# Optimization experiments

Hardware: AMD Instinct MI355X
Metric: run time of the kernel (lower is better)

Reference implementation:

```python
import jax, jax.numpy as jnp
import numpy as np

N_NODES = 50000
IN_CH = 128
HID = 128
N_EDGES = 800000


def _glorot(key, shape):
    fan_in, fan_out = shape[0], shape[1]
    lim = (6.0 / (fan_in + fan_out)) ** 0.5
    return jax.random.uniform(key, shape, jnp.float32, -lim, lim)


def setup_inputs() -> dict:
    key = jax.random.key(0)
    ks = jax.random.split(key, 8)
    x = jax.random.normal(ks[0], (N_NODES, IN_CH), jnp.float32)
    edge_index = jax.random.randint(ks[1], (2, N_EDGES), 0, N_NODES, jnp.int64)
    return {
        "x": x,
        "edge_index": edge_index,
        # SAGEConv1: lin_l (with bias) applied to mean-aggregated neighbors,
        # lin_r (no bias) applied to root features (PyG defaults, mean aggr)
        "W1l": _glorot(ks[2], (IN_CH, HID)),
        "b1l": jnp.zeros((HID,), jnp.float32),
        "W1r": _glorot(ks[3], (IN_CH, HID)),
        # SAGEConv2
        "W2l": _glorot(ks[4], (HID, HID)),
        "b2l": jnp.zeros((HID,), jnp.float32),
        "W2r": _glorot(ks[5], (HID, HID)),
        # final Linear(hidden, 1)
        "Wout": _glorot(ks[6], (HID, 1)),
        "bout": jnp.zeros((1,), jnp.float32),
    }


def _sage_conv(x, src, dst, Wl, bl, Wr, n_nodes):
    # gather source features along edges, mean-reduce into destinations
    msgs = x[src]                                                # [E, D]
    sums = jax.ops.segment_sum(msgs, dst, num_segments=n_nodes)  # [N, D]
    cnt = jax.ops.segment_sum(jnp.ones((src.shape[0], 1), x.dtype), dst,
                              num_segments=n_nodes)              # [N, 1]
    agg = sums / jnp.maximum(cnt, 1.0)
    return agg @ Wl + bl + x @ Wr


def reference(x, edge_index, W1l, b1l, W1r, W2l, b2l, W2r, Wout, bout):
    src, dst = edge_index[0], edge_index[1]
    n = x.shape[0]
    h = jax.nn.relu(_sage_conv(x, src, dst, W1l, b1l, W1r, n))
    h = jax.nn.relu(_sage_conv(h, src, dst, W2l, b2l, W2r, n))
    return (h @ Wout + bout).squeeze(-1)  # [N]
```

## Files before the change

kernel.cpp:

```cpp
#include <hip/hip_runtime.h>

#define D 128
#define LSTR 132
#define CAP 3072
#define NBLK 256

typedef __attribute__((ext_vector_type(8))) short short8;
typedef __attribute__((ext_vector_type(4))) float f32x4;

static __device__ __forceinline__ unsigned short f2bf(float f) {
    unsigned u = __float_as_uint(f);
    return (unsigned short)((u + 0x7fffu + ((u >> 16) & 1u)) >> 16);
}
static __device__ __forceinline__ float b2f(unsigned short u) {
    return __uint_as_float(((unsigned)u) << 16);
}


__global__ __launch_bounds__(256) void prep_hist_kernel(
    const float* __restrict__ x, const float* __restrict__ W1l,
    const float* __restrict__ W1r, const float* __restrict__ W2l,
    const float* __restrict__ W2r, unsigned* __restrict__ xb2,
    unsigned short* __restrict__ Bt1, unsigned short* __restrict__ Bt2,
    int NX2, const int* __restrict__ dst, int E, int nbins,
    unsigned* __restrict__ G) {
    const int t = threadIdx.x;
    if (blockIdx.x < NBLK) {
        __shared__ int h[2048];
        for (int i = t; i < nbins; i += 256) h[i] = 0;
        __syncthreads();
        const int per = (E + NBLK - 1) / NBLK;
        const int lo = blockIdx.x * per;
        const int hi = min(lo + per, E);
        for (int i = lo + t; i < hi; i += 256) atomicAdd(&h[dst[i] >> 5], 1);
        __syncthreads();
        for (int i = t; i < nbins; i += 256)
            G[(size_t)i * NBLK + blockIdx.x] = (unsigned)h[i];
        return;
    }
    const int i = (blockIdx.x - NBLK) * 256 + t;
    if (i < NX2) {
        const float2 v = *(const float2*)(x + 2 * (size_t)i);
        xb2[i] = (unsigned)f2bf(v.x) | ((unsigned)f2bf(v.y) << 16);
    } else if (i < NX2 + 2 * 32768) {
        const int j = i - NX2;
        const int which = j >> 15;
        const int jj = j & 32767;
        const int n = jj >> 8;
        const int k = jj & 255;
        const float* Wl = which ? W2l : W1l;
        const float* Wr = which ? W2r : W1r;
        const float w = (k < 128) ? Wl[k * 128 + n] : Wr[(k - 128) * 128 + n];
        (which ? Bt2 : Bt1)[jj] = f2bf(w);
    }
}

__global__ __launch_bounds__(256) void scanB_kernel(unsigned* __restrict__ G,
                                                    int nbins,
                                                    int* __restrict__ tot) {
    const int wave = threadIdx.x >> 6;
    const int lane = threadIdx.x & 63;
    const int bin = blockIdx.x * 4 + wave;
    if (bin >= nbins) return;
    unsigned* p = G + (size_t)bin * NBLK + lane * 4;
    uint4 v = *(uint4*)p;
    const unsigned s = v.x + v.y + v.z + v.w;
    unsigned sc = s;
#pragma unroll
    for (int off = 1; off < 64; off <<= 1) {
        const unsigned u = (unsigned)__shfl_up((int)sc, off, 64);
        if (lane >= off) sc += u;
    }
    const unsigned excl = sc - s;
    uint4 w;
    w.x = excl;
    w.y = excl + v.x;
    w.z = excl + v.x + v.y;
    w.w = excl + v.x + v.y + v.z;
    *(uint4*)p = w;
    if (lane == 63) tot[bin] = (int)(excl + s);
}

__global__ __launch_bounds__(1024) void scanC_kernel(
    const int* __restrict__ tot, int nbins, int* __restrict__ tile_base) {
    __shared__ int part[1024];
    const int t = threadIdx.x;
    const int chunk = (nbins + 1023) >> 10;
    const int lo = min(t * chunk, nbins);
    const int hi = min(lo + chunk, nbins);
    int s = 0;
    for (int i = lo; i < hi; ++i) s += tot[i];
    part[t] = s;
    __syncthreads();
    for (int off = 1; off < 1024; off <<= 1) {
        int add = (t >= off) ? part[t - off] : 0;
        __syncthreads();
        part[t] += add;
        __syncthreads();
    }
    int excl = (t == 0) ? 0 : part[t - 1];
    for (int i = lo; i < hi; ++i) {
        tile_base[i] = excl;
        excl += tot[i];
    }
    if (t == 1023) tile_base[nbins] = part[1023];
}

__global__ __launch_bounds__(256) void fillB_kernel(
    const int* __restrict__ src, const int* __restrict__ dst, int E,
    const unsigned* __restrict__ G, const int* __restrict__ tile_base,
    unsigned* __restrict__ csr, int nbins) {
    __shared__ int rank[2048];
    __shared__ int base[2048];
    const int t = threadIdx.x;
    for (int i = t; i < nbins; i += 256) {
        rank[i] = 0;
        base[i] = tile_base[i] + (int)G[(size_t)i * NBLK + blockIdx.x];
    }
    __syncthreads();
    const int per = (E + NBLK - 1) / NBLK;
    const int lo = blockIdx.x * per;
    const int hi = min(lo + per, E);
    for (int i = lo + t; i < hi; i += 256) {
        const int d = dst[i];
        const int bin = d >> 5;
        const int r = atomicAdd(&rank[bin], 1);
        csr[base[bin] + r] = (unsigned)src[i] | ((unsigned)d << 16);
    }
}

__global__ __launch_bounds__(256) void sortT_kernel(unsigned* __restrict__ csr,
                                                    const int* __restrict__
                                                        tile_base,
                                                    float* __restrict__ invL_g,
                                                    int N) {
    __shared__ unsigned sortedE[CAP];
    __shared__ int rowcnt[32];
    __shared__ int rowofs[32];
    const int b = blockIdx.x;
    const int i0 = b * 32;
    const int t = threadIdx.x;
    const int rs0 = tile_base[b];
    const int re0 = tile_base[b + 1];
    const int nE = re0 - rs0;

    if (t < 32) rowcnt[t] = 0;
    __syncthreads();
    for (int i = t; i < nE; i += 256)
        atomicAdd(&rowcnt[(csr[rs0 + i] >> 16) & 31], 1);
    __syncthreads();
    if (t < 32) {
        const int v = rowcnt[t];
        if (i0 + t < N) invL_g[i0 + t] = 1.0f / fmaxf((float)v, 1.0f);
        int s = v;
#pragma unroll
        for (int off = 1; off < 32; off <<= 1) {
            const int u = __shfl_up(s, off, 32);
            if ((t & 31) >= off) s += u;
        }
        rowofs[t] = s - v;
    }
    __syncthreads();
    if (nE <= CAP) {
        for (int i = t; i < nE; i += 256) {
            const unsigned p = csr[rs0 + i];
            const int k = atomicAdd(&rowofs[(p >> 16) & 31], 1);
            sortedE[k] = p;
        }
        __syncthreads();
        for (int i = t; i < nE; i += 256) csr[rs0 + i] = sortedE[i];
    }
}

template <bool HEAD>
__global__ __launch_bounds__(256) void sage_kernel(
    const unsigned short* __restrict__ xb, const unsigned* __restrict__ csr,
    const int* __restrict__ tile_base, const float* __restrict__ invL_g,
    const unsigned short* __restrict__ Bt,
    const float* __restrict__ bl, const float* __restrict__ Wout,
    const float* __restrict__ bout, unsigned short* __restrict__ hb_out,
    float* __restrict__ out, int N) {
    __shared__ float aggL[32 * LSTR];
    __shared__ float invL[32];
    __shared__ float redH[64];

    const int b = blockIdx.x;
    const int i0 = b * 32;
    const int t = threadIdx.x;
    const int g = t >> 5;
    const int l = t & 31;
    const int c4 = l << 2;

    for (int i = t; i < 32 * LSTR; i += 256) aggL[i] = 0.f;
    if (t < 32) invL[t] = (i0 + t < N) ? invL_g[i0 + t] : 1.0f;
    __syncthreads();

    const int rs0 = tile_base[b];
    const int re0 = tile_base[b + 1];
    const int nE = re0 - rs0;
    int e = rs0 + ((nE * g) >> 3);
    const int ee = rs0 + ((nE * (g + 1)) >> 3);

    float4 acc = make_float4(0.f, 0.f, 0.f, 0.f);
    int cur = (e < ee) ? (int)(csr[e] >> 16) - i0 : -1;

    auto load4 = [&](unsigned p) -> float4 {
        const ushort4 u =
            *(const ushort4*)(xb + (size_t)(p & 0xffffu) * D + c4);
        float4 v;
        v.x = b2f(u.x); v.y = b2f(u.y); v.z = b2f(u.z); v.w = b2f(u.w);
        return v;
    };
    auto step = [&](unsigned p, const float4& v) {
        const int r = (int)(p >> 16) - i0;
        if (r != cur) {
            float* q = aggL + cur * LSTR + c4;
            atomicAdd(q + 0, acc.x);
            atomicAdd(q + 1, acc.y);
            atomicAdd(q + 2, acc.z);
            atomicAdd(q + 3, acc.w);
            acc = make_float4(0.f, 0.f, 0.f, 0.f);
            cur = r;
        }
        acc.x += v.x; acc.y += v.y; acc.z += v.z; acc.w += v.w;
    };

    while (e + 8 <= ee) {
        const unsigned p0 = csr[e + 0], p1 = csr[e + 1];
        const unsigned p2 = csr[e + 2], p3 = csr[e + 3];
        const unsigned p4 = csr[e + 4], p5 = csr[e + 5];
        const unsigned p6 = csr[e + 6], p7 = csr[e + 7];
        const float4 v0 = load4(p0), v1 = load4(p1), v2 = load4(p2),
                     v3 = load4(p3), v4 = load4(p4), v5 = load4(p5),
                     v6 = load4(p6), v7 = load4(p7);
        step(p0, v0); step(p1, v1); step(p2, v2); step(p3, v3);
        step(p4, v4); step(p5, v5); step(p6, v6); step(p7, v7);
        e += 8;
    }
    while (e < ee) {
        const unsigned p = csr[e];
        step(p, load4(p));
        ++e;
    }
    if (cur >= 0) {
        float* q = aggL + cur * LSTR + c4;
        atomicAdd(q + 0, acc.x);
        atomicAdd(q + 1, acc.y);
        atomicAdd(q + 2, acc.z);
        atomicAdd(q + 3, acc.w);
    }
    __syncthreads();

    const int wave = t >> 6;
    const int lane = t & 63;
    const int ln = lane & 15;
    const int quad = lane >> 4;
    const int mtile = wave & 1;
    const int nt0 = (wave >> 1) * 4;
    const int mrow = mtile * 16 + ln;
    const int gmr = i0 + mrow;
    const float inv = invL[mrow];

    f32x4 acc4[4] = {f32x4{0.f, 0.f, 0.f, 0.f}, f32x4{0.f, 0.f, 0.f, 0.f},
                     f32x4{0.f, 0.f, 0.f, 0.f}, f32x4{0.f, 0.f, 0.f, 0.f}};

#pragma unroll
    for (int s = 0; s < 4; ++s) {
        const int kb = s * 32 + quad * 8;
        const float* ap = aggL + mrow * LSTR + kb;
        const float4 fa = *(const float4*)ap;
        const float4 fb = *(const float4*)(ap + 4);
        const short8 aA = {(short)f2bf(fa.x * inv), (short)f2bf(fa.y * inv),
                           (short)f2bf(fa.z * inv), (short)f2bf(fa.w * inv),
                           (short)f2bf(fb.x * inv), (short)f2bf(fb.y * inv),
                           (short)f2bf(fb.z * inv), (short)f2bf(fb.w * inv)};
        short8 aX = {0, 0, 0, 0, 0, 0, 0, 0};
        if (gmr < N) aX = *(const short8*)(xb + (size_t)gmr * D + kb);
#pragma unroll
        for (int nt = 0; nt < 4; ++nt) {
            const int n = (nt0 + nt) * 16 + ln;
            const short8 b1 = *(const short8*)(Bt + n * 256 + kb);
            const short8 b2 = *(const short8*)(Bt + n * 256 + 128 + kb);
            acc4[nt] = __builtin_amdgcn_mfma_f32_16x16x32_bf16(aA, b1, acc4[nt],
                                                               0, 0, 0);
            acc4[nt] = __builtin_amdgcn_mfma_f32_16x16x32_bf16(aX, b2, acc4[nt],
                                                               0, 0, 0);
        }
    }

    float biasv[4], woutv[4];
#pragma unroll
    for (int nt = 0; nt < 4; ++nt) {
        const int col = (nt0 + nt) * 16 + ln;
        biasv[nt] = bl[col];
        if (HEAD) woutv[nt] = Wout[col];
    }

    if (!HEAD) {
#pragma unroll
        for (int r = 0; r < 4; ++r) {
            const int gr = i0 + mtile * 16 + quad * 4 + r;
            if (gr < N) {
#pragma unroll
                for (int nt = 0; nt < 4; ++nt) {
                    const int col = (nt0 + nt) * 16 + ln;
                    const float v = fmaxf(acc4[nt][r] + biasv[nt], 0.f);
                    hb_out[(size_t)gr * D + col] = f2bf(v);
                }
            }
        }
    } else {
        const float b0 = bout[0];
#pragma unroll
        for (int r = 0; r < 4; ++r) {
            const int row = mtile * 16 + quad * 4 + r;
            float p = 0.f;
#pragma unroll
            for (int nt = 0; nt < 4; ++nt) {
                const float v = fmaxf(acc4[nt][r] + biasv[nt], 0.f);
                p += v * woutv[nt];
            }
            p += __shfl_xor(p, 1);
            p += __shfl_xor(p, 2);
            p += __shfl_xor(p, 4);
            p += __shfl_xor(p, 8);
            if (ln == 0) redH[row * 2 + (wave >> 1)] = p;
        }
        __syncthreads();
        if (t < 32) {
            const int gr = i0 + t;
            if (gr < N) out[gr] = redH[t * 2] + redH[t * 2 + 1] + b0;
        }
    }
}

extern "C" void kernel_launch(void* const* d_in, const int* in_sizes, int n_in,
                              void* d_out, int out_size, void* d_ws,
                              size_t ws_size, hipStream_t stream) {
    const float* x = (const float*)d_in[0];
    const int* ei = (const int*)d_in[1];
    const float* W1l = (const float*)d_in[2];
    const float* b1l = (const float*)d_in[3];
    const float* W1r = (const float*)d_in[4];
    const float* W2l = (const float*)d_in[5];
    const float* b2l = (const float*)d_in[6];
    const float* W2r = (const float*)d_in[7];
    const float* Wout = (const float*)d_in[8];
    const float* bout = (const float*)d_in[9];

    const int N = in_sizes[0] / D;
    const int E = in_sizes[1] / 2;
    const int* src = ei;
    const int* dst = ei + E;

    const int nbins = (N + 31) / 32;
    const size_t Npad = (size_t)((N + 255) & ~255);
    const size_t Epad = (size_t)((E + 255) & ~255);

    int* tot = (int*)d_ws;
    int* tile_base = tot + 2048;
    float* invL_g = (float*)(tile_base + 2052);
    unsigned* G = (unsigned*)(invL_g + Npad);
    unsigned* csr = G + (size_t)2048 * NBLK;
    unsigned short* xb = (unsigned short*)(csr + Epad);
    unsigned short* hb = xb + (size_t)N * D;
    unsigned short* Bt1 = hb + (size_t)N * D;
    unsigned short* Bt2 = Bt1 + 128 * 256;
    float* out = (float*)d_out;

    const int NX2 = N * D / 2;
    const int prep_blocks = (NX2 + 2 * 32768 + 255) / 256;

    prep_hist_kernel<<<NBLK + prep_blocks, 256, 0, stream>>>(
        x, W1l, W1r, W2l, W2r, (unsigned*)xb, Bt1, Bt2, NX2, dst, E, nbins, G);
    scanB_kernel<<<(nbins + 3) / 4, 256, 0, stream>>>(G, nbins, tot);
    scanC_kernel<<<1, 1024, 0, stream>>>(tot, nbins, tile_base);
    fillB_kernel<<<NBLK, 256, 0, stream>>>(src, dst, E, G, tile_base, csr,
                                           nbins);
    sortT_kernel<<<nbins, 256, 0, stream>>>(csr, tile_base, invL_g, N);

    sage_kernel<false><<<nbins, 256, 0, stream>>>(
        xb, csr, tile_base, invL_g, Bt1, b1l, nullptr, nullptr, hb, nullptr, N);
    sage_kernel<true><<<nbins, 256, 0, stream>>>(
        hb, csr, tile_base, invL_g, Bt2, b2l, Wout, bout, nullptr, out, N);
}
```

Measured before the change: 259.4 us.

## Simplify CSR build with global atomics and widen SAGE blocks to 512 threads

Replaces the per-block histogram matrix and its two-level scan with global atomic bin totals, then fills the CSR with one thread per edge using a global atomic cursor, dropping the scanB kernel. The SAGE kernels move to 512 threads per block, stage each tile's edge list in shared memory before gathering, and split the MFMA N-tiles over more waves. The x-to-bf16 conversion is widened to float4. The trade-offs are global atomic contention in the fill step, an extra memset, and more shared memory per block, which could limit occupancy.

```diff
diff --git a/kernel.cpp b/kernel.cpp
--- a/kernel.cpp
+++ b/kernel.cpp
@@ -12,38 +12,40 @@
     unsigned u = __float_as_uint(f);
     return (unsigned short)((u + 0x7fffu + ((u >> 16) & 1u)) >> 16);
 }
-static __device__ __forceinline__ float b2f(unsigned short u) {
-    return __uint_as_float(((unsigned)u) << 16);
-}
 
 
 __global__ __launch_bounds__(256) void prep_hist_kernel(
     const float* __restrict__ x, const float* __restrict__ W1l,
     const float* __restrict__ W1r, const float* __restrict__ W2l,
-    const float* __restrict__ W2r, unsigned* __restrict__ xb2,
+    const float* __restrict__ W2r, uint2* __restrict__ xb4,
     unsigned short* __restrict__ Bt1, unsigned short* __restrict__ Bt2,
-    int NX2, const int* __restrict__ dst, int E, int nbins,
-    unsigned* __restrict__ G) {
+    int NX4, const int* __restrict__ dst, int E, int nbins,
+    int* __restrict__ tot) {
     const int t = threadIdx.x;
     if (blockIdx.x < NBLK) {
         __shared__ int h[2048];
-        for (int i = t; i < nbins; i += 256) h[i] = 0;
+        for (int i = t; i < 2048; i += 256) h[i] = 0;
         __syncthreads();
         const int per = (E + NBLK - 1) / NBLK;
         const int lo = blockIdx.x * per;
         const int hi = min(lo + per, E);
         for (int i = lo + t; i < hi; i += 256) atomicAdd(&h[dst[i] >> 5], 1);
         __syncthreads();
-        for (int i = t; i < nbins; i += 256)
-            G[(size_t)i * NBLK + blockIdx.x] = (unsigned)h[i];
+        for (int i = t; i < nbins; i += 256) {
+            const int v = h[i];
+            if (v) atomicAdd(&tot[i], v);
+        }
         return;
     }
     const int i = (blockIdx.x - NBLK) * 256 + t;
-    if (i < NX2) {
-        const float2 v = *(const float2*)(x + 2 * (size_t)i);
-        xb2[i] = (unsigned)f2bf(v.x) | ((unsigned)f2bf(v.y) << 16);
-    } else if (i < NX2 + 2 * 32768) {
-        const int j = i - NX2;
+    if (i < NX4) {
+        const float4 v = *(const float4*)(x + 4 * (size_t)i);
+        uint2 o;
+        o.x = (unsigned)f2bf(v.x) | ((unsigned)f2bf(v.y) << 16);
+        o.y = (unsigned)f2bf(v.z) | ((unsigned)f2bf(v.w) << 16);
+        xb4[i] = o;
+    } else if (i < NX4 + 2 * 32768) {
+        const int j = i - NX4;
         const int which = j >> 15;
         const int jj = j & 32767;
         const int n = jj >> 8;
@@ -55,34 +57,9 @@
     }
 }
 
-__global__ __launch_bounds__(256) void scanB_kernel(unsigned* __restrict__ G,
-                                                    int nbins,
-                                                    int* __restrict__ tot) {
-    const int wave = threadIdx.x >> 6;
-    const int lane = threadIdx.x & 63;
-    const int bin = blockIdx.x * 4 + wave;
-    if (bin >= nbins) return;
-    unsigned* p = G + (size_t)bin * NBLK + lane * 4;
-    uint4 v = *(uint4*)p;
-    const unsigned s = v.x + v.y + v.z + v.w;
-    unsigned sc = s;
-#pragma unroll
-    for (int off = 1; off < 64; off <<= 1) {
-        const unsigned u = (unsigned)__shfl_up((int)sc, off, 64);
-        if (lane >= off) sc += u;
-    }
-    const unsigned excl = sc - s;
-    uint4 w;
-    w.x = excl;
-    w.y = excl + v.x;
-    w.z = excl + v.x + v.y;
-    w.w = excl + v.x + v.y + v.z;
-    *(uint4*)p = w;
-    if (lane == 63) tot[bin] = (int)(excl + s);
-}
-
 __global__ __launch_bounds__(1024) void scanC_kernel(
-    const int* __restrict__ tot, int nbins, int* __restrict__ tile_base) {
+    const int* __restrict__ tot, int nbins, int* __restrict__ tile_base,
+    int* __restrict__ cursor) {
     __shared__ int part[1024];
     const int t = threadIdx.x;
     const int chunk = (nbins + 1023) >> 10;
@@ -101,31 +78,20 @@
     int excl = (t == 0) ? 0 : part[t - 1];
     for (int i = lo; i < hi; ++i) {
         tile_base[i] = excl;
+        cursor[i] = excl;
         excl += tot[i];
     }
     if (t == 1023) tile_base[nbins] = part[1023];
 }
 
-__global__ __launch_bounds__(256) void fillB_kernel(
+__global__ __launch_bounds__(256) void fill_kernel(
     const int* __restrict__ src, const int* __restrict__ dst, int E,
-    const unsigned* __restrict__ G, const int* __restrict__ tile_base,
-    unsigned* __restrict__ csr, int nbins) {
-    __shared__ int rank[2048];
-    __shared__ int base[2048];
-    const int t = threadIdx.x;
-    for (int i = t; i < nbins; i += 256) {
-        rank[i] = 0;
-        base[i] = tile_base[i] + (int)G[(size_t)i * NBLK + blockIdx.x];
-    }
-    __syncthreads();
-    const int per = (E + NBLK - 1) / NBLK;
-    const int lo = blockIdx.x * per;
-    const int hi = min(lo + per, E);
-    for (int i = lo + t; i < hi; i += 256) {
+    int* __restrict__ cursor, unsigned* __restrict__ csr) {
+    const int i = blockIdx.x * 256 + threadIdx.x;
+    if (i < E) {
         const int d = dst[i];
-        const int bin = d >> 5;
-        const int r = atomicAdd(&rank[bin], 1);
-        csr[base[bin] + r] = (unsigned)src[i] | ((unsigned)d << 16);
+        const int pos = atomicAdd(&cursor[d >> 5], 1);
+        csr[pos] = (unsigned)src[i] | ((unsigned)d << 16);
     }
 }
 
@@ -173,7 +139,7 @@
 }
 
 template <bool HEAD>
-__global__ __launch_bounds__(256) void sage_kernel(
+__global__ __launch_bounds__(512) void sage_kernel(
     const unsigned short* __restrict__ xb, const unsigned* __restrict__ csr,
     const int* __restrict__ tile_base, const float* __restrict__ invL_g,
     const unsigned short* __restrict__ Bt,
@@ -181,8 +147,9 @@
     const float* __restrict__ bout, unsigned short* __restrict__ hb_out,
     float* __restrict__ out, int N) {
     __shared__ float aggL[32 * LSTR];
+    __shared__ unsigned csrL[CAP];
     __shared__ float invL[32];
-    __shared__ float redH[64];
+    __shared__ float redH[128];
 
     const int b = blockIdx.x;
     const int i0 = b * 32;
@@ -191,56 +158,68 @@
     const int l = t & 31;
     const int c4 = l << 2;
 
-    for (int i = t; i < 32 * LSTR; i += 256) aggL[i] = 0.f;
-    if (t < 32) invL[t] = (i0 + t < N) ? invL_g[i0 + t] : 1.0f;
-    __syncthreads();
-
     const int rs0 = tile_base[b];
     const int re0 = tile_base[b + 1];
     const int nE = re0 - rs0;
-    int e = rs0 + ((nE * g) >> 3);
-    const int ee = rs0 + ((nE * (g + 1)) >> 3);
+    const int nS = min(nE, CAP);
+
+    for (int i = t; i < 32 * LSTR; i += 512) aggL[i] = 0.f;
+    if (t < 32) invL[t] = (i0 + t < N) ? invL_g[i0 + t] : 1.0f;
+    for (int i = t; i < nS; i += 512) csrL[i] = csr[rs0 + i];
+    __syncthreads();
+
+    int e = (nS * g) >> 4;
+    const int ee = (nS * (g + 1)) >> 4;
 
     float4 acc = make_float4(0.f, 0.f, 0.f, 0.f);
-    int cur = (e < ee) ? (int)(csr[e] >> 16) - i0 : -1;
-
-    auto load4 = [&](unsigned p) -> float4 {
-        const ushort4 u =
-            *(const ushort4*)(xb + (size_t)(p & 0xffffu) * D + c4);
-        float4 v;
-        v.x = b2f(u.x); v.y = b2f(u.y); v.z = b2f(u.z); v.w = b2f(u.w);
-        return v;
+    int cur = -1;
+
+    auto ld = [&](unsigned p) -> uint2 {
+        return *(const uint2*)(xb + (size_t)(p & 0xffffu) * D + c4);
     };
-    auto step = [&](unsigned p, const float4& v) {
+    auto step = [&](unsigned p, uint2 u) {
         const int r = (int)(p >> 16) - i0;
         if (r != cur) {
-            float* q = aggL + cur * LSTR + c4;
-            atomicAdd(q + 0, acc.x);
-            atomicAdd(q + 1, acc.y);
-            atomicAdd(q + 2, acc.z);
-            atomicAdd(q + 3, acc.w);
+            if (cur >= 0) {
+                float* q = aggL + cur * LSTR + c4;
+                atomicAdd(q + 0, acc.x);
+                atomicAdd(q + 1, acc.y);
+                atomicAdd(q + 2, acc.z);
+                atomicAdd(q + 3, acc.w);
+            }
             acc = make_float4(0.f, 0.f, 0.f, 0.f);
             cur = r;
         }
-        acc.x += v.x; acc.y += v.y; acc.z += v.z; acc.w += v.w;
+        acc.x += __uint_as_float(u.x << 16);
+        acc.y += __uint_as_float(u.x & 0xffff0000u);
+        acc.z += __uint_as_float(u.y << 16);
+        acc.w += __uint_as_float(u.y & 0xffff0000u);
     };
 
     while (e + 8 <= ee) {
-        const unsigned p0 = csr[e + 0], p1 = csr[e + 1];
-        const unsigned p2 = csr[e + 2], p3 = csr[e + 3];
-        const unsigned p4 = csr[e + 4], p5 = csr[e + 5];
-        const unsigned p6 = csr[e + 6], p7 = csr[e + 7];
-        const float4 v0 = load4(p0), v1 = load4(p1), v2 = load4(p2),
-                     v3 = load4(p3), v4 = load4(p4), v5 = load4(p5),
-                     v6 = load4(p6), v7 = load4(p7);
+        const unsigned p0 = csrL[e + 0], p1 = csrL[e + 1];
+        const unsigned p2 = csrL[e + 2], p3 = csrL[e + 3];
+        const unsigned p4 = csrL[e + 4], p5 = csrL[e + 5];
+        const unsigned p6 = csrL[e + 6], p7 = csrL[e + 7];
+        const uint2 v0 = ld(p0), v1 = ld(p1), v2 = ld(p2), v3 = ld(p3),
+                    v4 = ld(p4), v5 = ld(p5), v6 = ld(p6), v7 = ld(p7);
         step(p0, v0); step(p1, v1); step(p2, v2); step(p3, v3);
         step(p4, v4); step(p5, v5); step(p6, v6); step(p7, v7);
         e += 8;
     }
     while (e < ee) {
-        const unsigned p = csr[e];
-        step(p, load4(p));
+        const unsigned p = csrL[e];
+        step(p, ld(p));
         ++e;
+    }
+    if (nE > CAP) {
+        const int extra = nE - CAP;
+        int e2 = CAP + ((extra * g) >> 4);
+        const int ee2 = CAP + ((extra * (g + 1)) >> 4);
+        for (; e2 < ee2; ++e2) {
+            const unsigned p = csr[rs0 + e2];
+            step(p, ld(p));
+        }
     }
     if (cur >= 0) {
         float* q = aggL + cur * LSTR + c4;
@@ -251,18 +230,17 @@
     }
     __syncthreads();
 
-    const int wave = t >> 6;
+    const int wv = t >> 6;
     const int lane = t & 63;
     const int ln = lane & 15;
     const int quad = lane >> 4;
-    const int mtile = wave & 1;
-    const int nt0 = (wave >> 1) * 4;
+    const int mtile = wv & 1;
+    const int nt0 = (wv >> 1) * 2;
     const int mrow = mtile * 16 + ln;
     const int gmr = i0 + mrow;
     const float inv = invL[mrow];
 
-    f32x4 acc4[4] = {f32x4{0.f, 0.f, 0.f, 0.f}, f32x4{0.f, 0.f, 0.f, 0.f},
-                     f32x4{0.f, 0.f, 0.f, 0.f}, f32x4{0.f, 0.f, 0.f, 0.f}};
+    f32x4 acc4[2] = {f32x4{0.f, 0.f, 0.f, 0.f}, f32x4{0.f, 0.f, 0.f, 0.f}};
 
 #pragma unroll
     for (int s = 0; s < 4; ++s) {
@@ -277,7 +255,7 @@
         short8 aX = {0, 0, 0, 0, 0, 0, 0, 0};
         if (gmr < N) aX = *(const short8*)(xb + (size_t)gmr * D + kb);
 #pragma unroll
-        for (int nt = 0; nt < 4; ++nt) {
+        for (int nt = 0; nt < 2; ++nt) {
             const int n = (nt0 + nt) * 16 + ln;
             const short8 b1 = *(const short8*)(Bt + n * 256 + kb);
             const short8 b2 = *(const short8*)(Bt + n * 256 + 128 + kb);
@@ -288,9 +266,9 @@
         }
     }
 
-    float biasv[4], woutv[4];
-#pragma unroll
-    for (int nt = 0; nt < 4; ++nt) {
+    float biasv[2], woutv[2];
+#pragma unroll
+    for (int nt = 0; nt < 2; ++nt) {
         const int col = (nt0 + nt) * 16 + ln;
         biasv[nt] = bl[col];
         if (HEAD) woutv[nt] = Wout[col];
@@ -302,7 +280,7 @@
             const int gr = i0 + mtile * 16 + quad * 4 + r;
             if (gr < N) {
 #pragma unroll
-                for (int nt = 0; nt < 4; ++nt) {
+                for (int nt = 0; nt < 2; ++nt) {
                     const int col = (nt0 + nt) * 16 + ln;
                     const float v = fmaxf(acc4[nt][r] + biasv[nt], 0.f);
                     hb_out[(size_t)gr * D + col] = f2bf(v);
@@ -316,7 +294,7 @@
             const int row = mtile * 16 + quad * 4 + r;
             float p = 0.f;
 #pragma unroll
-            for (int nt = 0; nt < 4; ++nt) {
+            for (int nt = 0; nt < 2; ++nt) {
                 const float v = fmaxf(acc4[nt][r] + biasv[nt], 0.f);
                 p += v * woutv[nt];
             }
@@ -324,12 +302,14 @@
             p += __shfl_xor(p, 2);
             p += __shfl_xor(p, 4);
             p += __shfl_xor(p, 8);
-            if (ln == 0) redH[row * 2 + (wave >> 1)] = p;
+            if (ln == 0) redH[row * 4 + (wv >> 1)] = p;
         }
         __syncthreads();
         if (t < 32) {
             const int gr = i0 + t;
-            if (gr < N) out[gr] = redH[t * 2] + redH[t * 2 + 1] + b0;
+            if (gr < N)
+                out[gr] = redH[t * 4] + redH[t * 4 + 1] + redH[t * 4 + 2] +
+                          redH[t * 4 + 3] + b0;
         }
     }
 }
@@ -359,28 +339,27 @@
 
     int* tot = (int*)d_ws;
     int* tile_base = tot + 2048;
-    float* invL_g = (float*)(tile_base + 2052);
-    unsigned* G = (unsigned*)(invL_g + Npad);
-    unsigned* csr = G + (size_t)2048 * NBLK;
+    int* cursor = tile_base + 2052;
+    float* invL_g = (float*)(cursor + 2048);
+    unsigned* csr = (unsigned*)(invL_g + Npad);
     unsigned short* xb = (unsigned short*)(csr + Epad);
     unsigned short* hb = xb + (size_t)N * D;
     unsigned short* Bt1 = hb + (size_t)N * D;
     unsigned short* Bt2 = Bt1 + 128 * 256;
     float* out = (float*)d_out;
 
-    const int NX2 = N * D / 2;
-    const int prep_blocks = (NX2 + 2 * 32768 + 255) / 256;
-
+    const int NX4 = N * D / 4;
+    const int prep_blocks = (NX4 + 2 * 32768 + 255) / 256;
+
+    hipMemsetAsync(tot, 0, 2048 * sizeof(int), stream);
     prep_hist_kernel<<<NBLK + prep_blocks, 256, 0, stream>>>(
-        x, W1l, W1r, W2l, W2r, (unsigned*)xb, Bt1, Bt2, NX2, dst, E, nbins, G);
-    scanB_kernel<<<(nbins + 3) / 4, 256, 0, stream>>>(G, nbins, tot);
-    scanC_kernel<<<1, 1024, 0, stream>>>(tot, nbins, tile_base);
-    fillB_kernel<<<NBLK, 256, 0, stream>>>(src, dst, E, G, tile_base, csr,
-                                           nbins);
+        x, W1l, W1r, W2l, W2r, (uint2*)xb, Bt1, Bt2, NX4, dst, E, nbins, tot);
+    scanC_kernel<<<1, 1024, 0, stream>>>(tot, nbins, tile_base, cursor);
+    fill_kernel<<<(E + 255) / 256, 256, 0, stream>>>(src, dst, E, cursor, csr);
     sortT_kernel<<<nbins, 256, 0, stream>>>(csr, tile_base, invL_g, N);
 
-    sage_kernel<false><<<nbins, 256, 0, stream>>>(
+    sage_kernel<false><<<nbins, 512, 0, stream>>>(
         xb, csr, tile_base, invL_g, Bt1, b1l, nullptr, nullptr, hb, nullptr, N);
-    sage_kernel<true><<<nbins, 256, 0, stream>>>(
+    sage_kernel<true><<<nbins, 512, 0, stream>>>(
         hb, csr, tile_base, invL_g, Bt2, b2l, Wout, bout, nullptr, out, N);
 }
```

Result: slower. 379.2 us (+46.2%).
